# Performance work log

Measured on AMD Instinct MI355X. Metric: run time of the kernel, lower is better.

The kernel has to match this reference:

```python
import jax, jax.numpy as jnp
import numpy as np

sp = jax.nn.softplus


def hip_block(x, W1, b1, W2, b2):
    # HIPResidual: out = a(L1(x)); out = a(L2(out) + x)
    h = sp(x @ W1 + b1)
    return sp(h @ W2 + b2 + x)


def res_stack(x, Ws1, bs1, Ws2, bs2):
    for i in range(Ws1.shape[0]):  # fixed small n_res=3
        x = hip_block(x, Ws1[i], bs1[i], Ws2[i], bs2[i])
    return x


def setup_inputs() -> dict:
    key = jax.random.key(0)
    ks = jax.random.split(key, 24)
    B, A, F, R, P, NRES = 64, 256, 80, 20, 393216, 3
    N = B * A
    s = 0.05
    inp = {
        "species": jax.random.randint(ks[0], (B, A), 0, 5),
        "features": jax.random.normal(ks[1], (N, F), jnp.float32),
        "radial_aev": jax.random.uniform(ks[2], (P, R), jnp.float32),
        "atom_index12": jax.random.randint(ks[3], (2, P), 0, N),
        "WI": jax.random.normal(ks[4], (F, F), jnp.float32) * s,
        "bI": jnp.zeros((F,), jnp.float32),
        "Wg": jax.random.normal(ks[5], (R, F), jnp.float32) * s,
        "bg": jnp.zeros((F,), jnp.float32),
        "WJ": jax.random.normal(ks[6], (F, F), jnp.float32) * s,
        "bJ": jnp.zeros((F,), jnp.float32),
        "iW1": jax.random.normal(ks[7], (NRES, F, F), jnp.float32) * s,
        "ib1": jnp.zeros((NRES, F), jnp.float32),
        "iW2": jax.random.normal(ks[8], (NRES, F, F), jnp.float32) * s,
        "ib2": jnp.zeros((NRES, F), jnp.float32),
        "gate": jnp.ones((F,), jnp.float32),
        "Wint": jax.random.normal(ks[9], (F, F), jnp.float32) * s,
        "bint": jnp.zeros((F,), jnp.float32),
        "aW1": jax.random.normal(ks[10], (NRES, F, F), jnp.float32) * s,
        "ab1": jnp.zeros((NRES, F), jnp.float32),
        "aW2": jax.random.normal(ks[11], (NRES, F, F), jnp.float32) * s,
        "ab2": jnp.zeros((NRES, F), jnp.float32),
        "oW1": jax.random.normal(ks[12], (NRES, F, F), jnp.float32) * s,
        "ob1": jnp.zeros((NRES, F), jnp.float32),
        "oW2": jax.random.normal(ks[13], (NRES, F, F), jnp.float32) * s,
        "ob2": jnp.zeros((NRES, F), jnp.float32),
        "Wout": jax.random.normal(ks[14], (F, 1), jnp.float32) * s,
        "bout": jnp.zeros((1,), jnp.float32),
    }
    return inp


def reference(species, features, radial_aev, atom_index12,
              WI, bI, Wg, bg, WJ, bJ,
              iW1, ib1, iW2, ib2,
              gate, Wint, bint,
              aW1, ab1, aW2, ab2,
              oW1, ob1, oW2, ob2,
              Wout, bout):
    B, A = species.shape
    N, F = features.shape
    # dummy-atom mask (species == -1 rows are excluded in the original via
    # index_select/index_add; all per-atom ops are row-wise so masking is exact)
    mask = (species.reshape(-1) != -1).astype(features.dtype)[:, None]  # [N,1]

    # pair message: gather -> gated small MLP -> scatter-add
    f12 = features[atom_index12]                       # [2,P,F]
    aev_term = radial_aev @ Wg + bg                    # [P,F]
    fmsg = sp(sp(f12) @ WJ + bJ)                       # [2,P,F]
    pair_msg = aev_term[None] * fmsg                   # [2,P,F]

    proto = jnp.zeros_like(features).at[atom_index12.reshape(-1)].add(
        pair_msg.reshape(-1, F))
    proto = proto + (features @ WI + bI) * mask        # no-interaction term

    message = res_stack(proto, iW1, ib1, iW2, ib2)
    nd = features * gate[None, :] + sp(message) @ Wint + bint
    nd = res_stack(nd, aW1, ab1, aW2, ab2)
    energies = (sp(res_stack(nd, oW1, ob1, oW2, ob2)) @ Wout + bout)[:, 0]

    out_energies = (energies * mask[:, 0]).reshape(B, A)
    out_features = nd * mask
    return out_energies, out_features
```

## Files before the change

### kernel.cpp

```cpp
#include <hip/hip_runtime.h>
#include <hip/hip_bf16.h>

#define FDIM 80
#define RDIM 20
#define NSLOT 6
#define LDP  104
#define WROW 96
#define AROWS 32

#define FIX_SCALE 512.0f
#define FIX_INV   0.001953125f

typedef float  f32x4  __attribute__((ext_vector_type(4)));
typedef short  bf16x8 __attribute__((ext_vector_type(8)));

__device__ __forceinline__ float sp_f(float x){
  float e = __expf(-fabsf(x));
  return fmaxf(x, 0.f) + __logf(1.f + e);
}
__device__ __forceinline__ __hip_bfloat16 tob(float x){ return __float2bfloat16(x); }

struct WPtrs { const float* p[21]; };

__global__ __launch_bounds__(256) void prep_weights(WPtrs wp, __hip_bfloat16* __restrict__ wt){
  const float* W = wp.p[blockIdx.x];
  __hip_bfloat16* dst = wt + (size_t)blockIdx.x * FDIM * WROW;
  for (int i = threadIdx.x; i < FDIM * WROW; i += 256){
    int j = i / WROW, k = i - j * WROW;
    dst[i] = __float2bfloat16(k < FDIM ? W[k * FDIM + j] : 0.f);
  }
}

__global__ __launch_bounds__(256) void scatter_p16(const float* __restrict__ aev,
    const int* __restrict__ idx12, unsigned long long* __restrict__ R6u, int P)
{
  int g = blockIdx.x * 256 + threadIdx.x;
  if (g >= P * NSLOT) return;
  int p = g / NSLOT, s = g - p * NSLOT;
  unsigned long long v;
  if (s < 5){
    float4 a = ((const float4*)(aev + (size_t)p * RDIM))[s];
    unsigned long long f0 = (unsigned long long)__float2uint_rn(a.x * FIX_SCALE);
    unsigned long long f1 = (unsigned long long)__float2uint_rn(a.y * FIX_SCALE);
    unsigned long long f2 = (unsigned long long)__float2uint_rn(a.z * FIX_SCALE);
    unsigned long long f3 = (unsigned long long)__float2uint_rn(a.w * FIX_SCALE);
    v = f0 | (f1 << 16) | (f2 << 32) | (f3 << 48);
  } else {
    v = 512ULL;
  }
  int i1 = idx12[p], i2 = idx12[P + p];
  atomicAdd(&R6u[(size_t)i1 * NSLOT + s], v);
  atomicAdd(&R6u[(size_t)i2 * NSLOT + s], v);
}

#define TPB2 320
__global__ __launch_bounds__(TPB2) void aevt_kernel(
    const unsigned long long* __restrict__ R6u,
    const float* __restrict__ Wg, const float* __restrict__ bg,
    float* __restrict__ S, int N)
{
  __shared__ float Rl[64][4 * NSLOT];
  const int t = threadIdx.x;
  const int base = blockIdx.x * 64;
  for (int i = t; i < 64 * NSLOT; i += TPB2){
    int u = i / NSLOT, s = i - u * NSLOT;
    unsigned long long v = R6u[(size_t)(base + u) * NSLOT + s];
    #pragma unroll
    for (int f = 0; f < 4; f++)
      Rl[u][4*s + f] = (float)((unsigned int)(v >> (16*f)) & 0xffffu) * FIX_INV;
  }
  const int j = t % FDIM, rg = t / FDIM;
  float wc[RDIM];
  #pragma unroll
  for (int r = 0; r < RDIM; r++) wc[r] = Wg[r * FDIM + j];
  float bgj = bg[j];
  __syncthreads();
  #pragma unroll 1
  for (int ui = 0; ui < 16; ui++){
    int u = rg + 4 * ui;
    float acc = Rl[u][RDIM] * bgj;
    #pragma unroll
    for (int r = 0; r < RDIM; r++) acc += Rl[u][r] * wc[r];
    S[(size_t)(base + u) * FDIM + j] = acc;
  }
}

__device__ __forceinline__ void mfma_layer2(f32x4 acc[2],
    const __hip_bfloat16 (*in)[LDP], int j0, int kb, int nt,
    const __hip_bfloat16* __restrict__ wtm, const float* __restrict__ bias)
{
  const __hip_bfloat16* wp = &wtm[(size_t)(16*nt + j0) * WROW + kb];
  bf16x8 b0 = *(const bf16x8*)(const void*)(wp);
  bf16x8 b1 = *(const bf16x8*)(const void*)(wp + 32);
  bf16x8 b2 = *(const bf16x8*)(const void*)(wp + 64);
  float bv = bias[16*nt + j0];
  #pragma unroll
  for (int s = 0; s < 2; s++){
    const __hip_bfloat16* ap = &in[16*s + j0][kb];
    bf16x8 a0 = *(const bf16x8*)(const void*)(ap);
    bf16x8 a1 = *(const bf16x8*)(const void*)(ap + 32);
    bf16x8 a2 = *(const bf16x8*)(const void*)(ap + 64);
    acc[s] = (f32x4){bv, bv, bv, bv};
    acc[s] = __builtin_amdgcn_mfma_f32_16x16x32_bf16(a0, b0, acc[s], 0, 0, 0);
    acc[s] = __builtin_amdgcn_mfma_f32_16x16x32_bf16(a1, b1, acc[s], 0, 0, 0);
    acc[s] = __builtin_amdgcn_mfma_f32_16x16x32_bf16(a2, b2, acc[s], 0, 0, 0);
  }
}

__device__ __forceinline__ void res2(f32x4 cur[2],
    __hip_bfloat16 (*bA)[LDP], __hip_bfloat16 (*bB)[LDP],
    int j0, int kb, int g, int nt,
    const __hip_bfloat16* __restrict__ w1, const float* __restrict__ b1,
    const __hip_bfloat16* __restrict__ w2, const float* __restrict__ b2)
{
  f32x4 acc[2];
  const int col = 16*nt + j0;
  mfma_layer2(acc, bA, j0, kb, nt, w1, b1);
  #pragma unroll
  for (int s = 0; s < 2; s++){
    int r0 = 16*s + g*4;
    #pragma unroll
    for (int i = 0; i < 4; i++) bB[r0 + i][col] = tob(sp_f(acc[s][i]));
  }
  __syncthreads();
  mfma_layer2(acc, bB, j0, kb, nt, w2, b2);
  #pragma unroll
  for (int s = 0; s < 2; s++){
    int r0 = 16*s + g*4;
    #pragma unroll
    for (int i = 0; i < 4; i++){
      cur[s][i] = sp_f(acc[s][i] + cur[s][i]);
      bA[r0 + i][col] = tob(cur[s][i]);
    }
  }
  __syncthreads();
}

__global__ __launch_bounds__(320) void atom_mfma(
    const int*   __restrict__ species,
    const float* __restrict__ features,
    const float* __restrict__ S,
    const __hip_bfloat16* __restrict__ wt,
    const float* __restrict__ bJ, const float* __restrict__ bI,
    const float* __restrict__ ib1, const float* __restrict__ ib2,
    const float* __restrict__ gate, const float* __restrict__ bint,
    const float* __restrict__ ab1, const float* __restrict__ ab2,
    const float* __restrict__ ob1, const float* __restrict__ ob2,
    const float* __restrict__ Wout, const float* __restrict__ bout,
    float* __restrict__ out_e, float* __restrict__ out_f)
{
  __shared__ __align__(16) __hip_bfloat16 bufA[AROWS][LDP];
  __shared__ __align__(16) __hip_bfloat16 bufB[AROWS][LDP];
  __shared__ __align__(16) __hip_bfloat16 xfb[AROWS][LDP];
  __shared__ float mskl[AROWS];
  __shared__ float evp[5][AROWS];

  const int t    = threadIdx.x;
  const int lane = t & 63;
  const int nt   = t >> 6;
  const int base = blockIdx.x * AROWS;

  for (int i = t; i < AROWS * FDIM; i += 320){
    int row = i / FDIM, col = i - row * FDIM;
    float v = features[(size_t)(base + row) * FDIM + col];
    xfb [row][col] = tob(v);
    bufA[row][col] = tob(sp_f(v));
  }
  for (int i = t; i < 3 * AROWS * 16; i += 320){
    int b = i / (AROWS * 16), rem = i % (AROWS * 16);
    int row = rem >> 4, col = FDIM + (rem & 15);
    if      (b == 0) bufA[row][col] = tob(0.f);
    else if (b == 1) bufB[row][col] = tob(0.f);
    else             xfb [row][col] = tob(0.f);
  }
  if (t < AROWS) mskl[t] = (species[base + t] != -1) ? 1.f : 0.f;
  __syncthreads();

  const int j0  = lane & 15;
  const int g   = lane >> 4;
  const int kb  = g * 8;
  const int col = 16*nt + j0;

  f32x4 cur[2];

  {
    f32x4 accJ[2], accI[2];
    mfma_layer2(accJ, bufA, j0, kb, nt, wt + (size_t)0*FDIM*WROW, bJ);
    mfma_layer2(accI, xfb , j0, kb, nt, wt + (size_t)1*FDIM*WROW, bI);
    __syncthreads();
    #pragma unroll
    for (int s = 0; s < 2; s++){
      int r0 = 16*s + g*4;
      #pragma unroll
      for (int i = 0; i < 4; i++){
        float Sv = S[(size_t)(base + r0 + i) * FDIM + col];
        float m  = mskl[r0 + i];
        cur[s][i] = sp_f(accJ[s][i]) * Sv + accI[s][i] * m;
        bufA[r0 + i][col] = tob(cur[s][i]);
      }
    }
  }
  __syncthreads();

  #pragma unroll 1
  for (int ir = 0; ir < 3; ir++)
    res2(cur, bufA, bufB, j0, kb, g, nt,
         wt + (size_t)(3+2*ir)*FDIM*WROW, ib1 + ir*FDIM,
         wt + (size_t)(4+2*ir)*FDIM*WROW, ib2 + ir*FDIM);

  {
    #pragma unroll
    for (int s = 0; s < 2; s++){
      int r0 = 16*s + g*4;
      #pragma unroll
      for (int i = 0; i < 4; i++) bufB[r0 + i][col] = tob(sp_f(cur[s][i]));
    }
    __syncthreads();
    f32x4 acc[2];
    mfma_layer2(acc, bufB, j0, kb, nt, wt + (size_t)2*FDIM*WROW, bint);
    float gj = gate[col];
    #pragma unroll
    for (int s = 0; s < 2; s++){
      int r0 = 16*s + g*4;
      #pragma unroll
      for (int i = 0; i < 4; i++){
        float xv = __bfloat162float(xfb[r0 + i][col]);
        cur[s][i] = xv * gj + acc[s][i];
        bufA[r0 + i][col] = tob(cur[s][i]);
      }
    }
    __syncthreads();
  }

  #pragma unroll 1
  for (int ir = 0; ir < 3; ir++)
    res2(cur, bufA, bufB, j0, kb, g, nt,
         wt + (size_t)(9+2*ir)*FDIM*WROW, ab1 + ir*FDIM,
         wt + (size_t)(10+2*ir)*FDIM*WROW, ab2 + ir*FDIM);

  #pragma unroll
  for (int s = 0; s < 2; s++){
    int r0 = 16*s + g*4;
    #pragma unroll
    for (int i = 0; i < 4; i++)
      out_f[(size_t)(base + r0 + i) * FDIM + col] = cur[s][i] * mskl[r0 + i];
  }

  #pragma unroll 1
  for (int ir = 0; ir < 3; ir++)
    res2(cur, bufA, bufB, j0, kb, g, nt,
         wt + (size_t)(15+2*ir)*FDIM*WROW, ob1 + ir*FDIM,
         wt + (size_t)(16+2*ir)*FDIM*WROW, ob2 + ir*FDIM);

  {
    float wv = Wout[col];
    float ev[2][4];
    #pragma unroll
    for (int s = 0; s < 2; s++)
      #pragma unroll
      for (int i = 0; i < 4; i++) ev[s][i] = sp_f(cur[s][i]) * wv;
    #pragma unroll
    for (int off = 1; off < 16; off <<= 1){
      #pragma unroll
      for (int s = 0; s < 2; s++)
        #pragma unroll
        for (int i = 0; i < 4; i++) ev[s][i] += __shfl_xor(ev[s][i], off);
    }
    if (j0 == 0){
      #pragma unroll
      for (int s = 0; s < 2; s++)
        #pragma unroll
        for (int i = 0; i < 4; i++) evp[nt][16*s + g*4 + i] = ev[s][i];
    }
  }
  __syncthreads();
  if (t < AROWS)
    out_e[base + t] = (evp[0][t] + evp[1][t] + evp[2][t] + evp[3][t] + evp[4][t]
                       + bout[0]) * mskl[t];
}

extern "C" void kernel_launch(void* const* d_in, const int* in_sizes, int n_in,
                              void* d_out, int out_size, void* d_ws, size_t ws_size,
                              hipStream_t stream) {
  const int*   species  = (const int*)  d_in[0];
  const float* features = (const float*)d_in[1];
  const float* aev      = (const float*)d_in[2];
  const int*   idx12    = (const int*)  d_in[3];
  const float* WI   = (const float*)d_in[4];  const float* bI   = (const float*)d_in[5];
  const float* Wg   = (const float*)d_in[6];  const float* bg   = (const float*)d_in[7];
  const float* WJ   = (const float*)d_in[8];  const float* bJ   = (const float*)d_in[9];
  const float* iW1  = (const float*)d_in[10]; const float* ib1  = (const float*)d_in[11];
  const float* iW2  = (const float*)d_in[12]; const float* ib2  = (const float*)d_in[13];
  const float* gate = (const float*)d_in[14];
  const float* Wint = (const float*)d_in[15]; const float* bint = (const float*)d_in[16];
  const float* aW1  = (const float*)d_in[17]; const float* ab1  = (const float*)d_in[18];
  const float* aW2  = (const float*)d_in[19]; const float* ab2  = (const float*)d_in[20];
  const float* oW1  = (const float*)d_in[21]; const float* ob1  = (const float*)d_in[22];
  const float* oW2  = (const float*)d_in[23]; const float* ob2  = (const float*)d_in[24];
  const float* Wout = (const float*)d_in[25]; const float* bout = (const float*)d_in[26];

  const int N = in_sizes[1] / FDIM;
  const int P = in_sizes[2] / RDIM;

  unsigned long long* R6u = (unsigned long long*)d_ws;
  float* S = (float*)(R6u + (size_t)N * NSLOT);
  __hip_bfloat16* wt = (__hip_bfloat16*)(S + (size_t)N * FDIM);

  float* out_e = (float*)d_out;
  float* out_f = out_e + N;

  hipMemsetAsync(R6u, 0, (size_t)N * NSLOT * sizeof(unsigned long long), stream);

  WPtrs wp;
  wp.p[0] = WJ; wp.p[1] = WI; wp.p[2] = Wint;
  for (int ir = 0; ir < 3; ir++){
    wp.p[3  + 2*ir] = iW1 + ir*FDIM*FDIM; wp.p[4  + 2*ir] = iW2 + ir*FDIM*FDIM;
    wp.p[9  + 2*ir] = aW1 + ir*FDIM*FDIM; wp.p[10 + 2*ir] = aW2 + ir*FDIM*FDIM;
    wp.p[15 + 2*ir] = oW1 + ir*FDIM*FDIM; wp.p[16 + 2*ir] = oW2 + ir*FDIM*FDIM;
  }
  prep_weights<<<21, 256, 0, stream>>>(wp, wt);

  scatter_p16<<<((size_t)P * NSLOT + 255) / 256, 256, 0, stream>>>(aev, idx12, R6u, P);
  aevt_kernel<<<(N + 63) / 64, TPB2, 0, stream>>>(R6u, Wg, bg, S, N);

  atom_mfma<<<(N + AROWS - 1) / AROWS, 320, 0, stream>>>(species, features, S, wt,
      bJ, bI, ib1, ib2, gate, bint, ab1, ab2, ob1, ob2, Wout, bout, out_e, out_f);
}
```

Before: 114.5 us.

## Fuse AEV projection into atom kernel and prefetch next-layer weights into registers

```diff
diff --git a/kernel.cpp b/kernel.cpp
--- a/kernel.cpp
+++ b/kernel.cpp
@@ -53,69 +53,46 @@
   atomicAdd(&R6u[(size_t)i2 * NSLOT + s], v);
 }
 
-#define TPB2 320
-__global__ __launch_bounds__(TPB2) void aevt_kernel(
-    const unsigned long long* __restrict__ R6u,
-    const float* __restrict__ Wg, const float* __restrict__ bg,
-    float* __restrict__ S, int N)
+struct WF { bf16x8 b0, b1, b2; float bias; };
+
+__device__ __forceinline__ WF loadWF(const __hip_bfloat16* __restrict__ wb,
+                                     int slot, const float* __restrict__ bias, int row){
+  WF w;
+  const __hip_bfloat16* p = wb + (size_t)slot * (FDIM * WROW);
+  w.b0 = *(const bf16x8*)(const void*)(p);
+  w.b1 = *(const bf16x8*)(const void*)(p + 32);
+  w.b2 = *(const bf16x8*)(const void*)(p + 64);
+  w.bias = bias[row];
+  return w;
+}
+
+__device__ __forceinline__ void mfmaL(f32x4 acc[2],
+    const __hip_bfloat16 (*in)[LDP], int j0, int kb, const WF& w)
 {
-  __shared__ float Rl[64][4 * NSLOT];
-  const int t = threadIdx.x;
-  const int base = blockIdx.x * 64;
-  for (int i = t; i < 64 * NSLOT; i += TPB2){
-    int u = i / NSLOT, s = i - u * NSLOT;
-    unsigned long long v = R6u[(size_t)(base + u) * NSLOT + s];
-    #pragma unroll
-    for (int f = 0; f < 4; f++)
-      Rl[u][4*s + f] = (float)((unsigned int)(v >> (16*f)) & 0xffffu) * FIX_INV;
-  }
-  const int j = t % FDIM, rg = t / FDIM;
-  float wc[RDIM];
-  #pragma unroll
-  for (int r = 0; r < RDIM; r++) wc[r] = Wg[r * FDIM + j];
-  float bgj = bg[j];
-  __syncthreads();
-  #pragma unroll 1
-  for (int ui = 0; ui < 16; ui++){
-    int u = rg + 4 * ui;
-    float acc = Rl[u][RDIM] * bgj;
-    #pragma unroll
-    for (int r = 0; r < RDIM; r++) acc += Rl[u][r] * wc[r];
-    S[(size_t)(base + u) * FDIM + j] = acc;
-  }
-}
-
-__device__ __forceinline__ void mfma_layer2(f32x4 acc[2],
-    const __hip_bfloat16 (*in)[LDP], int j0, int kb, int nt,
-    const __hip_bfloat16* __restrict__ wtm, const float* __restrict__ bias)
-{
-  const __hip_bfloat16* wp = &wtm[(size_t)(16*nt + j0) * WROW + kb];
-  bf16x8 b0 = *(const bf16x8*)(const void*)(wp);
-  bf16x8 b1 = *(const bf16x8*)(const void*)(wp + 32);
-  bf16x8 b2 = *(const bf16x8*)(const void*)(wp + 64);
-  float bv = bias[16*nt + j0];
   #pragma unroll
   for (int s = 0; s < 2; s++){
     const __hip_bfloat16* ap = &in[16*s + j0][kb];
     bf16x8 a0 = *(const bf16x8*)(const void*)(ap);
     bf16x8 a1 = *(const bf16x8*)(const void*)(ap + 32);
     bf16x8 a2 = *(const bf16x8*)(const void*)(ap + 64);
-    acc[s] = (f32x4){bv, bv, bv, bv};
-    acc[s] = __builtin_amdgcn_mfma_f32_16x16x32_bf16(a0, b0, acc[s], 0, 0, 0);
-    acc[s] = __builtin_amdgcn_mfma_f32_16x16x32_bf16(a1, b1, acc[s], 0, 0, 0);
-    acc[s] = __builtin_amdgcn_mfma_f32_16x16x32_bf16(a2, b2, acc[s], 0, 0, 0);
-  }
-}
-
-__device__ __forceinline__ void res2(f32x4 cur[2],
+    acc[s] = (f32x4){w.bias, w.bias, w.bias, w.bias};
+    acc[s] = __builtin_amdgcn_mfma_f32_16x16x32_bf16(a0, w.b0, acc[s], 0, 0, 0);
+    acc[s] = __builtin_amdgcn_mfma_f32_16x16x32_bf16(a1, w.b1, acc[s], 0, 0, 0);
+    acc[s] = __builtin_amdgcn_mfma_f32_16x16x32_bf16(a2, w.b2, acc[s], 0, 0, 0);
+  }
+}
+
+__device__ __forceinline__ void resblk(f32x4 cur[2],
     __hip_bfloat16 (*bA)[LDP], __hip_bfloat16 (*bB)[LDP],
-    int j0, int kb, int g, int nt,
-    const __hip_bfloat16* __restrict__ w1, const float* __restrict__ b1,
-    const __hip_bfloat16* __restrict__ w2, const float* __restrict__ b2)
+    int j0, int kb, int g, int col,
+    WF& w1, WF& w2,
+    const __hip_bfloat16* __restrict__ wb, int row,
+    int pf1, const float* __restrict__ pf1b,
+    int pf2, const float* __restrict__ pf2b)
 {
   f32x4 acc[2];
-  const int col = 16*nt + j0;
-  mfma_layer2(acc, bA, j0, kb, nt, w1, b1);
+  mfmaL(acc, bA, j0, kb, w1);
+  w1 = loadWF(wb, pf1, pf1b, row);
   #pragma unroll
   for (int s = 0; s < 2; s++){
     int r0 = 16*s + g*4;
@@ -123,7 +100,8 @@
     for (int i = 0; i < 4; i++) bB[r0 + i][col] = tob(sp_f(acc[s][i]));
   }
   __syncthreads();
-  mfma_layer2(acc, bB, j0, kb, nt, w2, b2);
+  mfmaL(acc, bB, j0, kb, w2);
+  w2 = loadWF(wb, pf2, pf2b, row);
   #pragma unroll
   for (int s = 0; s < 2; s++){
     int r0 = 16*s + g*4;
@@ -136,11 +114,12 @@
   __syncthreads();
 }
 
-__global__ __launch_bounds__(320) void atom_mfma(
+__global__ __launch_bounds__(320, 4) void atom_mfma(
     const int*   __restrict__ species,
     const float* __restrict__ features,
-    const float* __restrict__ S,
+    const unsigned long long* __restrict__ R6u,
     const __hip_bfloat16* __restrict__ wt,
+    const float* __restrict__ Wg, const float* __restrict__ bg,
     const float* __restrict__ bJ, const float* __restrict__ bI,
     const float* __restrict__ ib1, const float* __restrict__ ib2,
     const float* __restrict__ gate, const float* __restrict__ bint,
@@ -152,6 +131,7 @@
   __shared__ __align__(16) __hip_bfloat16 bufA[AROWS][LDP];
   __shared__ __align__(16) __hip_bfloat16 bufB[AROWS][LDP];
   __shared__ __align__(16) __hip_bfloat16 xfb[AROWS][LDP];
+  __shared__ float Rl[AROWS][4 * NSLOT];
   __shared__ float mskl[AROWS];
   __shared__ float evp[5][AROWS];
 
@@ -160,55 +140,81 @@
   const int nt   = t >> 6;
   const int base = blockIdx.x * AROWS;
 
-  for (int i = t; i < AROWS * FDIM; i += 320){
-    int row = i / FDIM, col = i - row * FDIM;
-    float v = features[(size_t)(base + row) * FDIM + col];
-    xfb [row][col] = tob(v);
-    bufA[row][col] = tob(sp_f(v));
-  }
-  for (int i = t; i < 3 * AROWS * 16; i += 320){
-    int b = i / (AROWS * 16), rem = i % (AROWS * 16);
-    int row = rem >> 4, col = FDIM + (rem & 15);
-    if      (b == 0) bufA[row][col] = tob(0.f);
-    else if (b == 1) bufB[row][col] = tob(0.f);
-    else             xfb [row][col] = tob(0.f);
-  }
-  if (t < AROWS) mskl[t] = (species[base + t] != -1) ? 1.f : 0.f;
-  __syncthreads();
-
   const int j0  = lane & 15;
   const int g   = lane >> 4;
   const int kb  = g * 8;
   const int col = 16*nt + j0;
+  const int row = col;
+  const __hip_bfloat16* wb = wt + (size_t)row * WROW + kb;
+
+  float wgc[RDIM];
+  #pragma unroll
+  for (int r = 0; r < RDIM; r++) wgc[r] = Wg[r * FDIM + col];
+  const float bgv = bg[col];
+
+  for (int i = t; i < AROWS * FDIM; i += 320){
+    int rr = i / FDIM, cc = i - rr * FDIM;
+    float v = features[(size_t)(base + rr) * FDIM + cc];
+    xfb [rr][cc] = tob(v);
+    bufA[rr][cc] = tob(sp_f(v));
+  }
+  for (int i = t; i < 3 * AROWS * 16; i += 320){
+    int b = i / (AROWS * 16), rem = i % (AROWS * 16);
+    int rr = rem >> 4, cc = FDIM + (rem & 15);
+    if      (b == 0) bufA[rr][cc] = tob(0.f);
+    else if (b == 1) bufB[rr][cc] = tob(0.f);
+    else             xfb [rr][cc] = tob(0.f);
+  }
+  if (t < AROWS * NSLOT){
+    int u = t / NSLOT, s5 = t - u * NSLOT;
+    unsigned long long v = R6u[(size_t)(base + u) * NSLOT + s5];
+    #pragma unroll
+    for (int f = 0; f < 4; f++)
+      Rl[u][4*s5 + f] = (float)((unsigned int)(v >> (16*f)) & 0xffffu) * FIX_INV;
+  }
+  if (t < AROWS) mskl[t] = (species[base + t] != -1) ? 1.f : 0.f;
+  __syncthreads();
+
+  f32x4 Sreg[2];
+  #pragma unroll
+  for (int s = 0; s < 2; s++){
+    #pragma unroll
+    for (int i = 0; i < 4; i++){
+      int rr = 16*s + g*4 + i;
+      float a = Rl[rr][RDIM] * bgv;
+      #pragma unroll
+      for (int r = 0; r < RDIM; r++) a += Rl[rr][r] * wgc[r];
+      Sreg[s][i] = a;
+    }
+  }
 
   f32x4 cur[2];
 
   {
-    f32x4 accJ[2], accI[2];
-    mfma_layer2(accJ, bufA, j0, kb, nt, wt + (size_t)0*FDIM*WROW, bJ);
-    mfma_layer2(accI, xfb , j0, kb, nt, wt + (size_t)1*FDIM*WROW, bI);
+    WF wA = loadWF(wb, 0, bJ, row);
+    WF wB = loadWF(wb, 1, bI, row);
+    f32x4 aJ[2], aI[2];
+    mfmaL(aJ, bufA, j0, kb, wA);  wA = loadWF(wb, 3, ib1, row);
+    mfmaL(aI, xfb , j0, kb, wB);  wB = loadWF(wb, 4, ib2, row);
     __syncthreads();
     #pragma unroll
     for (int s = 0; s < 2; s++){
       int r0 = 16*s + g*4;
       #pragma unroll
       for (int i = 0; i < 4; i++){
-        float Sv = S[(size_t)(base + r0 + i) * FDIM + col];
-        float m  = mskl[r0 + i];
-        cur[s][i] = sp_f(accJ[s][i]) * Sv + accI[s][i] * m;
+        cur[s][i] = sp_f(aJ[s][i]) * Sreg[s][i] + aI[s][i] * mskl[r0 + i];
         bufA[r0 + i][col] = tob(cur[s][i]);
       }
     }
-  }
-  __syncthreads();
-
-  #pragma unroll 1
-  for (int ir = 0; ir < 3; ir++)
-    res2(cur, bufA, bufB, j0, kb, g, nt,
-         wt + (size_t)(3+2*ir)*FDIM*WROW, ib1 + ir*FDIM,
-         wt + (size_t)(4+2*ir)*FDIM*WROW, ib2 + ir*FDIM);
-
-  {
+    __syncthreads();
+
+    resblk(cur, bufA, bufB, j0, kb, g, col, wA, wB, wb, row,
+           5, ib1 + FDIM,     6, ib2 + FDIM);
+    resblk(cur, bufA, bufB, j0, kb, g, col, wA, wB, wb, row,
+           7, ib1 + 2*FDIM,   8, ib2 + 2*FDIM);
+    resblk(cur, bufA, bufB, j0, kb, g, col, wA, wB, wb, row,
+           2, bint,           9, ab1);
+
     #pragma unroll
     for (int s = 0; s < 2; s++){
       int r0 = 16*s + g*4;
@@ -216,41 +222,46 @@
       for (int i = 0; i < 4; i++) bufB[r0 + i][col] = tob(sp_f(cur[s][i]));
     }
     __syncthreads();
-    f32x4 acc[2];
-    mfma_layer2(acc, bufB, j0, kb, nt, wt + (size_t)2*FDIM*WROW, bint);
-    float gj = gate[col];
+    {
+      f32x4 acc[2];
+      mfmaL(acc, bufB, j0, kb, wA);
+      wA = loadWF(wb, 10, ab2, row);
+      float gj = gate[col];
+      #pragma unroll
+      for (int s = 0; s < 2; s++){
+        int r0 = 16*s + g*4;
+        #pragma unroll
+        for (int i = 0; i < 4; i++){
+          float xv = __bfloat162float(xfb[r0 + i][col]);
+          cur[s][i] = xv * gj + acc[s][i];
+          bufA[r0 + i][col] = tob(cur[s][i]);
+        }
+      }
+    }
+    __syncthreads();
+
+    resblk(cur, bufA, bufB, j0, kb, g, col, wB, wA, wb, row,
+           11, ab1 + FDIM,    12, ab2 + FDIM);
+    resblk(cur, bufA, bufB, j0, kb, g, col, wB, wA, wb, row,
+           13, ab1 + 2*FDIM,  14, ab2 + 2*FDIM);
+    resblk(cur, bufA, bufB, j0, kb, g, col, wB, wA, wb, row,
+           15, ob1,           16, ob2);
+
     #pragma unroll
     for (int s = 0; s < 2; s++){
       int r0 = 16*s + g*4;
       #pragma unroll
-      for (int i = 0; i < 4; i++){
-        float xv = __bfloat162float(xfb[r0 + i][col]);
-        cur[s][i] = xv * gj + acc[s][i];
-        bufA[r0 + i][col] = tob(cur[s][i]);
-      }
-    }
-    __syncthreads();
-  }
-
-  #pragma unroll 1
-  for (int ir = 0; ir < 3; ir++)
-    res2(cur, bufA, bufB, j0, kb, g, nt,
-         wt + (size_t)(9+2*ir)*FDIM*WROW, ab1 + ir*FDIM,
-         wt + (size_t)(10+2*ir)*FDIM*WROW, ab2 + ir*FDIM);
-
-  #pragma unroll
-  for (int s = 0; s < 2; s++){
-    int r0 = 16*s + g*4;
-    #pragma unroll
-    for (int i = 0; i < 4; i++)
-      out_f[(size_t)(base + r0 + i) * FDIM + col] = cur[s][i] * mskl[r0 + i];
-  }
-
-  #pragma unroll 1
-  for (int ir = 0; ir < 3; ir++)
-    res2(cur, bufA, bufB, j0, kb, g, nt,
-         wt + (size_t)(15+2*ir)*FDIM*WROW, ob1 + ir*FDIM,
-         wt + (size_t)(16+2*ir)*FDIM*WROW, ob2 + ir*FDIM);
+      for (int i = 0; i < 4; i++)
+        out_f[(size_t)(base + r0 + i) * FDIM + col] = cur[s][i] * mskl[r0 + i];
+    }
+
+    resblk(cur, bufA, bufB, j0, kb, g, col, wB, wA, wb, row,
+           17, ob1 + FDIM,    18, ob2 + FDIM);
+    resblk(cur, bufA, bufB, j0, kb, g, col, wB, wA, wb, row,
+           19, ob1 + 2*FDIM,  20, ob2 + 2*FDIM);
+    resblk(cur, bufA, bufB, j0, kb, g, col, wB, wA, wb, row,
+           0, bJ,             0, bJ);
+  }
 
   {
     float wv = Wout[col];
@@ -303,8 +314,7 @@
   const int P = in_sizes[2] / RDIM;
 
   unsigned long long* R6u = (unsigned long long*)d_ws;
-  float* S = (float*)(R6u + (size_t)N * NSLOT);
-  __hip_bfloat16* wt = (__hip_bfloat16*)(S + (size_t)N * FDIM);
+  __hip_bfloat16* wt = (__hip_bfloat16*)(R6u + (size_t)N * NSLOT);
 
   float* out_e = (float*)d_out;
   float* out_f = out_e + N;
@@ -321,8 +331,8 @@
   prep_weights<<<21, 256, 0, stream>>>(wp, wt);
 
   scatter_p16<<<((size_t)P * NSLOT + 255) / 256, 256, 0, stream>>>(aev, idx12, R6u, P);
-  aevt_kernel<<<(N + 63) / 64, TPB2, 0, stream>>>(R6u, Wg, bg, S, N);
-
-  atom_mfma<<<(N + AROWS - 1) / AROWS, 320, 0, stream>>>(species, features, S, wt,
-      bJ, bI, ib1, ib2, gate, bint, ab1, ab2, ob1, ob2, Wout, bout, out_e, out_f);
-}
+
+  atom_mfma<<<(N + AROWS - 1) / AROWS, 320, 0, stream>>>(species, features, R6u, wt,
+      Wg, bg, bJ, bI, ib1, ib2, gate, bint, ab1, ab2, ob1, ob2, Wout, bout,
+      out_e, out_f);
+}
```

Result: faster. 107.0 us (-6.6%).

## Fuse AEV projection into atom kernel and give each wave private rows

Applied to the files above, without the earlier changes.

```diff
diff --git a/kernel.cpp b/kernel.cpp
--- a/kernel.cpp
+++ b/kernel.cpp
@@ -4,9 +4,8 @@
 #define FDIM 80
 #define RDIM 20
 #define NSLOT 6
-#define LDP  104
+#define LDSW 104
 #define WROW 96
-#define AROWS 32
 
 #define FIX_SCALE 512.0f
 #define FIX_INV   0.001953125f
@@ -53,94 +52,69 @@
   atomicAdd(&R6u[(size_t)i2 * NSLOT + s], v);
 }
 
-#define TPB2 320
-__global__ __launch_bounds__(TPB2) void aevt_kernel(
-    const unsigned long long* __restrict__ R6u,
-    const float* __restrict__ Wg, const float* __restrict__ bg,
-    float* __restrict__ S, int N)
-{
-  __shared__ float Rl[64][4 * NSLOT];
-  const int t = threadIdx.x;
-  const int base = blockIdx.x * 64;
-  for (int i = t; i < 64 * NSLOT; i += TPB2){
-    int u = i / NSLOT, s = i - u * NSLOT;
-    unsigned long long v = R6u[(size_t)(base + u) * NSLOT + s];
-    #pragma unroll
-    for (int f = 0; f < 4; f++)
-      Rl[u][4*s + f] = (float)((unsigned int)(v >> (16*f)) & 0xffffu) * FIX_INV;
-  }
-  const int j = t % FDIM, rg = t / FDIM;
-  float wc[RDIM];
-  #pragma unroll
-  for (int r = 0; r < RDIM; r++) wc[r] = Wg[r * FDIM + j];
-  float bgj = bg[j];
-  __syncthreads();
-  #pragma unroll 1
-  for (int ui = 0; ui < 16; ui++){
-    int u = rg + 4 * ui;
-    float acc = Rl[u][RDIM] * bgj;
-    #pragma unroll
-    for (int r = 0; r < RDIM; r++) acc += Rl[u][r] * wc[r];
-    S[(size_t)(base + u) * FDIM + j] = acc;
-  }
-}
-
-__device__ __forceinline__ void mfma_layer2(f32x4 acc[2],
-    const __hip_bfloat16 (*in)[LDP], int j0, int kb, int nt,
-    const __hip_bfloat16* __restrict__ wtm, const float* __restrict__ bias)
-{
-  const __hip_bfloat16* wp = &wtm[(size_t)(16*nt + j0) * WROW + kb];
-  bf16x8 b0 = *(const bf16x8*)(const void*)(wp);
-  bf16x8 b1 = *(const bf16x8*)(const void*)(wp + 32);
-  bf16x8 b2 = *(const bf16x8*)(const void*)(wp + 64);
-  float bv = bias[16*nt + j0];
-  #pragma unroll
-  for (int s = 0; s < 2; s++){
-    const __hip_bfloat16* ap = &in[16*s + j0][kb];
-    bf16x8 a0 = *(const bf16x8*)(const void*)(ap);
-    bf16x8 a1 = *(const bf16x8*)(const void*)(ap + 32);
-    bf16x8 a2 = *(const bf16x8*)(const void*)(ap + 64);
-    acc[s] = (f32x4){bv, bv, bv, bv};
-    acc[s] = __builtin_amdgcn_mfma_f32_16x16x32_bf16(a0, b0, acc[s], 0, 0, 0);
-    acc[s] = __builtin_amdgcn_mfma_f32_16x16x32_bf16(a1, b1, acc[s], 0, 0, 0);
-    acc[s] = __builtin_amdgcn_mfma_f32_16x16x32_bf16(a2, b2, acc[s], 0, 0, 0);
-  }
-}
-
-__device__ __forceinline__ void res2(f32x4 cur[2],
-    __hip_bfloat16 (*bA)[LDP], __hip_bfloat16 (*bB)[LDP],
-    int j0, int kb, int g, int nt,
-    const __hip_bfloat16* __restrict__ w1, const float* __restrict__ b1,
-    const __hip_bfloat16* __restrict__ w2, const float* __restrict__ b2)
-{
-  f32x4 acc[2];
-  const int col = 16*nt + j0;
-  mfma_layer2(acc, bA, j0, kb, nt, w1, b1);
-  #pragma unroll
-  for (int s = 0; s < 2; s++){
-    int r0 = 16*s + g*4;
-    #pragma unroll
-    for (int i = 0; i < 4; i++) bB[r0 + i][col] = tob(sp_f(acc[s][i]));
-  }
-  __syncthreads();
-  mfma_layer2(acc, bB, j0, kb, nt, w2, b2);
-  #pragma unroll
-  for (int s = 0; s < 2; s++){
-    int r0 = 16*s + g*4;
+struct WS { bf16x8 b[5][3]; float bias[5]; };
+
+__device__ __forceinline__ void loadWS(WS& w, const __hip_bfloat16* __restrict__ wt,
+    int slot, const float* __restrict__ bp, int j0, int kb)
+{
+  #pragma unroll
+  for (int q = 0; q < 5; q++){
+    const __hip_bfloat16* p = wt + ((size_t)slot * FDIM + 16*q + j0) * WROW + kb;
+    #pragma unroll
+    for (int ks = 0; ks < 3; ks++)
+      w.b[q][ks] = *(const bf16x8*)(const void*)(p + 32*ks);
+    w.bias[q] = bp[16*q + j0];
+  }
+}
+
+__device__ __forceinline__ void mmA(f32x4 acc[5],
+    const __hip_bfloat16 (*in)[LDSW], int j0, int kb, const WS& w)
+{
+  const __hip_bfloat16* ap = &in[j0][kb];
+  bf16x8 a0 = *(const bf16x8*)(const void*)(ap);
+  bf16x8 a1 = *(const bf16x8*)(const void*)(ap + 32);
+  bf16x8 a2 = *(const bf16x8*)(const void*)(ap + 64);
+  #pragma unroll
+  for (int q = 0; q < 5; q++) acc[q] = (f32x4){w.bias[q], w.bias[q], w.bias[q], w.bias[q]};
+  #pragma unroll
+  for (int q = 0; q < 5; q++) acc[q] = __builtin_amdgcn_mfma_f32_16x16x32_bf16(a0, w.b[q][0], acc[q], 0, 0, 0);
+  #pragma unroll
+  for (int q = 0; q < 5; q++) acc[q] = __builtin_amdgcn_mfma_f32_16x16x32_bf16(a1, w.b[q][1], acc[q], 0, 0, 0);
+  #pragma unroll
+  for (int q = 0; q < 5; q++) acc[q] = __builtin_amdgcn_mfma_f32_16x16x32_bf16(a2, w.b[q][2], acc[q], 0, 0, 0);
+}
+
+__device__ __forceinline__ void resblk(f32x4 cur[5],
+    __hip_bfloat16 (*act)[LDSW], int j0, int kb, int g,
+    WS& w1, WS& w2, const __hip_bfloat16* __restrict__ wt,
+    int s1n, const float* __restrict__ b1n,
+    int s2n, const float* __restrict__ b2n)
+{
+  f32x4 acc[5];
+  mmA(acc, act, j0, kb, w1);
+  loadWS(w1, wt, s1n, b1n, j0, kb);
+  #pragma unroll
+  for (int q = 0; q < 5; q++)
+    #pragma unroll
+    for (int i = 0; i < 4; i++)
+      act[g*4 + i][16*q + j0] = tob(sp_f(acc[q][i]));
+  mmA(acc, act, j0, kb, w2);
+  loadWS(w2, wt, s2n, b2n, j0, kb);
+  #pragma unroll
+  for (int q = 0; q < 5; q++)
     #pragma unroll
     for (int i = 0; i < 4; i++){
-      cur[s][i] = sp_f(acc[s][i] + cur[s][i]);
-      bA[r0 + i][col] = tob(cur[s][i]);
+      cur[q][i] = sp_f(acc[q][i] + cur[q][i]);
+      act[g*4 + i][16*q + j0] = tob(cur[q][i]);
     }
-  }
-  __syncthreads();
-}
-
-__global__ __launch_bounds__(320) void atom_mfma(
+}
+
+__global__ __launch_bounds__(256, 1) void atom_mfma(
     const int*   __restrict__ species,
     const float* __restrict__ features,
-    const float* __restrict__ S,
+    const unsigned long long* __restrict__ R6u,
     const __hip_bfloat16* __restrict__ wt,
+    const float* __restrict__ Wg, const float* __restrict__ bg,
     const float* __restrict__ bJ, const float* __restrict__ bI,
     const float* __restrict__ ib1, const float* __restrict__ ib2,
     const float* __restrict__ gate, const float* __restrict__ bint,
@@ -149,134 +123,152 @@
     const float* __restrict__ Wout, const float* __restrict__ bout,
     float* __restrict__ out_e, float* __restrict__ out_f)
 {
-  __shared__ __align__(16) __hip_bfloat16 bufA[AROWS][LDP];
-  __shared__ __align__(16) __hip_bfloat16 bufB[AROWS][LDP];
-  __shared__ __align__(16) __hip_bfloat16 xfb[AROWS][LDP];
-  __shared__ float mskl[AROWS];
-  __shared__ float evp[5][AROWS];
+  __shared__ __align__(16) __hip_bfloat16 actS[4][16][LDSW];
+  __shared__ __align__(16) __hip_bfloat16 xfbS[4][16][LDSW];
+  __shared__ float RlS[4][16][4 * NSLOT];
+  __shared__ float WgL[RDIM + 1][FDIM];
 
   const int t    = threadIdx.x;
   const int lane = t & 63;
-  const int nt   = t >> 6;
-  const int base = blockIdx.x * AROWS;
-
-  for (int i = t; i < AROWS * FDIM; i += 320){
-    int row = i / FDIM, col = i - row * FDIM;
-    float v = features[(size_t)(base + row) * FDIM + col];
-    xfb [row][col] = tob(v);
-    bufA[row][col] = tob(sp_f(v));
-  }
-  for (int i = t; i < 3 * AROWS * 16; i += 320){
-    int b = i / (AROWS * 16), rem = i % (AROWS * 16);
-    int row = rem >> 4, col = FDIM + (rem & 15);
-    if      (b == 0) bufA[row][col] = tob(0.f);
-    else if (b == 1) bufB[row][col] = tob(0.f);
-    else             xfb [row][col] = tob(0.f);
-  }
-  if (t < AROWS) mskl[t] = (species[base + t] != -1) ? 1.f : 0.f;
+  const int w    = t >> 6;
+  const int base = blockIdx.x * 64 + w * 16;
+
+  __hip_bfloat16 (*act)[LDSW] = actS[w];
+  __hip_bfloat16 (*xfb)[LDSW] = xfbS[w];
+  float (*Rl)[4 * NSLOT] = RlS[w];
+
+  const int j0 = lane & 15;
+  const int g  = lane >> 4;
+  const int kb = g * 8;
+
+  for (int i = t; i < (RDIM + 1) * FDIM; i += 256){
+    int r = i / FDIM, c = i - r * FDIM;
+    WgL[r][c] = (r < RDIM) ? Wg[r * FDIM + c] : bg[c];
+  }
+  #pragma unroll
+  for (int it = 0; it < 20; it++){
+    int idx = it * 64 + lane;
+    int row = idx / FDIM, c = idx - row * FDIM;
+    float v = features[(size_t)(base + row) * FDIM + c];
+    xfb[row][c] = tob(v);
+    act[row][c] = tob(sp_f(v));
+  }
+  #pragma unroll
+  for (int it = 0; it < 8; it++){
+    int idx = it * 64 + lane;
+    int row = (idx >> 4) & 15, c = FDIM + (idx & 15);
+    if (it < 4) act[row][c] = tob(0.f);
+    else        xfb[row][c] = tob(0.f);
+  }
+  #pragma unroll
+  for (int it = 0; it < 2; it++){
+    int idx = it * 64 + lane;
+    if (idx < 16 * NSLOT){
+      int u = idx / NSLOT, s = idx - u * NSLOT;
+      unsigned long long v = R6u[(size_t)(base + u) * NSLOT + s];
+      #pragma unroll
+      for (int f = 0; f < 4; f++)
+        Rl[u][4*s + f] = (float)((unsigned int)(v >> (16*f)) & 0xffffu) * FIX_INV;
+    }
+  }
+  float msk[4];
+  #pragma unroll
+  for (int i = 0; i < 4; i++)
+    msk[i] = (species[base + g*4 + i] != -1) ? 1.f : 0.f;
+  float greg[5], wo5[5];
+  #pragma unroll
+  for (int q = 0; q < 5; q++){ greg[q] = gate[16*q + j0]; wo5[q] = Wout[16*q + j0]; }
+
   __syncthreads();
 
-  const int j0  = lane & 15;
-  const int g   = lane >> 4;
-  const int kb  = g * 8;
-  const int col = 16*nt + j0;
-
-  f32x4 cur[2];
+  WS wA, wB;
+  loadWS(wA, wt, 0, bJ, j0, kb);
+  loadWS(wB, wt, 1, bI, j0, kb);
+
+  f32x4 Sreg[5];
+  #pragma unroll
+  for (int q = 0; q < 5; q++) Sreg[q] = (f32x4){0.f, 0.f, 0.f, 0.f};
+  for (int r = 0; r <= RDIM; r++){
+    float rv0 = Rl[g*4+0][r], rv1 = Rl[g*4+1][r], rv2 = Rl[g*4+2][r], rv3 = Rl[g*4+3][r];
+    #pragma unroll
+    for (int q = 0; q < 5; q++){
+      float wv = WgL[r][16*q + j0];
+      Sreg[q][0] += rv0 * wv; Sreg[q][1] += rv1 * wv;
+      Sreg[q][2] += rv2 * wv; Sreg[q][3] += rv3 * wv;
+    }
+  }
+
+  f32x4 cur[5];
 
   {
-    f32x4 accJ[2], accI[2];
-    mfma_layer2(accJ, bufA, j0, kb, nt, wt + (size_t)0*FDIM*WROW, bJ);
-    mfma_layer2(accI, xfb , j0, kb, nt, wt + (size_t)1*FDIM*WROW, bI);
-    __syncthreads();
-    #pragma unroll
-    for (int s = 0; s < 2; s++){
-      int r0 = 16*s + g*4;
+    f32x4 accJ[5], accI[5];
+    mmA(accJ, act, j0, kb, wA);
+    loadWS(wA, wt, 3, ib1, j0, kb);
+    mmA(accI, xfb, j0, kb, wB);
+    loadWS(wB, wt, 4, ib2, j0, kb);
+    #pragma unroll
+    for (int q = 0; q < 5; q++)
       #pragma unroll
       for (int i = 0; i < 4; i++){
-        float Sv = S[(size_t)(base + r0 + i) * FDIM + col];
-        float m  = mskl[r0 + i];
-        cur[s][i] = sp_f(accJ[s][i]) * Sv + accI[s][i] * m;
-        bufA[r0 + i][col] = tob(cur[s][i]);
+        cur[q][i] = sp_f(accJ[q][i]) * Sreg[q][i] + accI[q][i] * msk[i];
+        act[g*4 + i][16*q + j0] = tob(cur[q][i]);
       }
+  }
+
+  resblk(cur, act, j0, kb, g, wA, wB, wt, 5, ib1 + FDIM,   6, ib2 + FDIM);
+  resblk(cur, act, j0, kb, g, wA, wB, wt, 7, ib1 + 2*FDIM, 8, ib2 + 2*FDIM);
+  resblk(cur, act, j0, kb, g, wA, wB, wt, 2, bint,         9, ab1);
+
+  {
+    #pragma unroll
+    for (int q = 0; q < 5; q++)
+      #pragma unroll
+      for (int i = 0; i < 4; i++)
+        act[g*4 + i][16*q + j0] = tob(sp_f(cur[q][i]));
+    f32x4 acc[5];
+    mmA(acc, act, j0, kb, wA);
+    loadWS(wA, wt, 10, ab2, j0, kb);
+    #pragma unroll
+    for (int q = 0; q < 5; q++)
+      #pragma unroll
+      for (int i = 0; i < 4; i++){
+        float xv = __bfloat162float(xfb[g*4 + i][16*q + j0]);
+        cur[q][i] = xv * greg[q] + acc[q][i];
+        act[g*4 + i][16*q + j0] = tob(cur[q][i]);
+      }
+  }
+
+  resblk(cur, act, j0, kb, g, wB, wA, wt, 11, ab1 + FDIM,   12, ab2 + FDIM);
+  resblk(cur, act, j0, kb, g, wB, wA, wt, 13, ab1 + 2*FDIM, 14, ab2 + 2*FDIM);
+  resblk(cur, act, j0, kb, g, wB, wA, wt, 15, ob1,          16, ob2);
+
+  #pragma unroll
+  for (int q = 0; q < 5; q++)
+    #pragma unroll
+    for (int i = 0; i < 4; i++)
+      out_f[(size_t)(base + g*4 + i) * FDIM + 16*q + j0] = cur[q][i] * msk[i];
+
+  resblk(cur, act, j0, kb, g, wB, wA, wt, 17, ob1 + FDIM,   18, ob2 + FDIM);
+  resblk(cur, act, j0, kb, g, wB, wA, wt, 19, ob1 + 2*FDIM, 20, ob2 + 2*FDIM);
+  resblk(cur, act, j0, kb, g, wB, wA, wt, 0,  bJ,           0,  bJ);
+
+  {
+    f32x4 ev = (f32x4){0.f, 0.f, 0.f, 0.f};
+    #pragma unroll
+    for (int q = 0; q < 5; q++)
+      #pragma unroll
+      for (int i = 0; i < 4; i++) ev[i] += sp_f(cur[q][i]) * wo5[q];
+    #pragma unroll
+    for (int off = 1; off < 16; off <<= 1)
+      #pragma unroll
+      for (int i = 0; i < 4; i++) ev[i] += __shfl_xor(ev[i], off);
+    if (j0 == 0){
+      float b0 = bout[0];
+      #pragma unroll
+      for (int i = 0; i < 4; i++)
+        out_e[base + g*4 + i] = (ev[i] + b0) * msk[i];
     }
   }
-  __syncthreads();
-
-  #pragma unroll 1
-  for (int ir = 0; ir < 3; ir++)
-    res2(cur, bufA, bufB, j0, kb, g, nt,
-         wt + (size_t)(3+2*ir)*FDIM*WROW, ib1 + ir*FDIM,
-         wt + (size_t)(4+2*ir)*FDIM*WROW, ib2 + ir*FDIM);
-
-  {
-    #pragma unroll
-    for (int s = 0; s < 2; s++){
-      int r0 = 16*s + g*4;
-      #pragma unroll
-      for (int i = 0; i < 4; i++) bufB[r0 + i][col] = tob(sp_f(cur[s][i]));
-    }
-    __syncthreads();
-    f32x4 acc[2];
-    mfma_layer2(acc, bufB, j0, kb, nt, wt + (size_t)2*FDIM*WROW, bint);
-    float gj = gate[col];
-    #pragma unroll
-    for (int s = 0; s < 2; s++){
-      int r0 = 16*s + g*4;
-      #pragma unroll
-      for (int i = 0; i < 4; i++){
-        float xv = __bfloat162float(xfb[r0 + i][col]);
-        cur[s][i] = xv * gj + acc[s][i];
-        bufA[r0 + i][col] = tob(cur[s][i]);
-      }
-    }
-    __syncthreads();
-  }
-
-  #pragma unroll 1
-  for (int ir = 0; ir < 3; ir++)
-    res2(cur, bufA, bufB, j0, kb, g, nt,
-         wt + (size_t)(9+2*ir)*FDIM*WROW, ab1 + ir*FDIM,
-         wt + (size_t)(10+2*ir)*FDIM*WROW, ab2 + ir*FDIM);
-
-  #pragma unroll
-  for (int s = 0; s < 2; s++){
-    int r0 = 16*s + g*4;
-    #pragma unroll
-    for (int i = 0; i < 4; i++)
-      out_f[(size_t)(base + r0 + i) * FDIM + col] = cur[s][i] * mskl[r0 + i];
-  }
-
-  #pragma unroll 1
-  for (int ir = 0; ir < 3; ir++)
-    res2(cur, bufA, bufB, j0, kb, g, nt,
-         wt + (size_t)(15+2*ir)*FDIM*WROW, ob1 + ir*FDIM,
-         wt + (size_t)(16+2*ir)*FDIM*WROW, ob2 + ir*FDIM);
-
-  {
-    float wv = Wout[col];
-    float ev[2][4];
-    #pragma unroll
-    for (int s = 0; s < 2; s++)
-      #pragma unroll
-      for (int i = 0; i < 4; i++) ev[s][i] = sp_f(cur[s][i]) * wv;
-    #pragma unroll
-    for (int off = 1; off < 16; off <<= 1){
-      #pragma unroll
-      for (int s = 0; s < 2; s++)
-        #pragma unroll
-        for (int i = 0; i < 4; i++) ev[s][i] += __shfl_xor(ev[s][i], off);
-    }
-    if (j0 == 0){
-      #pragma unroll
-      for (int s = 0; s < 2; s++)
-        #pragma unroll
-        for (int i = 0; i < 4; i++) evp[nt][16*s + g*4 + i] = ev[s][i];
-    }
-  }
-  __syncthreads();
-  if (t < AROWS)
-    out_e[base + t] = (evp[0][t] + evp[1][t] + evp[2][t] + evp[3][t] + evp[4][t]
-                       + bout[0]) * mskl[t];
 }
 
 extern "C" void kernel_launch(void* const* d_in, const int* in_sizes, int n_in,
@@ -303,8 +295,7 @@
   const int P = in_sizes[2] / RDIM;
 
   unsigned long long* R6u = (unsigned long long*)d_ws;
-  float* S = (float*)(R6u + (size_t)N * NSLOT);
-  __hip_bfloat16* wt = (__hip_bfloat16*)(S + (size_t)N * FDIM);
+  __hip_bfloat16* wt = (__hip_bfloat16*)(R6u + (size_t)N * NSLOT);
 
   float* out_e = (float*)d_out;
   float* out_f = out_e + N;
@@ -321,8 +312,8 @@
   prep_weights<<<21, 256, 0, stream>>>(wp, wt);
 
   scatter_p16<<<((size_t)P * NSLOT + 255) / 256, 256, 0, stream>>>(aev, idx12, R6u, P);
-  aevt_kernel<<<(N + 63) / 64, TPB2, 0, stream>>>(R6u, Wg, bg, S, N);
-
-  atom_mfma<<<(N + AROWS - 1) / AROWS, 320, 0, stream>>>(species, features, S, wt,
-      bJ, bI, ib1, ib2, gate, bint, ab1, ab2, ob1, ob2, Wout, bout, out_e, out_f);
-}
+
+  atom_mfma<<<N / 64, 256, 0, stream>>>(species, features, R6u, wt,
+      Wg, bg, bJ, bI, ib1, ib2, gate, bint, ab1, ab2, ob1, ob2, Wout, bout,
+      out_e, out_f);
+}
```

Result: no change. 115.8 us (+1.1%).
